# Performance work log

Measured on AMD Instinct MI355X. Metric: run time of the kernel, lower is better.

## Reference

```python
import jax, jax.numpy as jnp
import numpy as np

B, N, X, Y, W1, W2 = 2, 6, 8, 8, 8, 8
DIM, HEADS, DHEAD = 128, 4, 32
HD = HEADS * DHEAD
EPS = 1e-5


def setup_inputs() -> dict:
    key = jax.random.key(0)
    ks = jax.random.split(key, 12)
    d = {}
    d['q'] = jax.random.normal(ks[0], (B, N, X, Y, W1, W2, DIM), jnp.float32)
    d['k'] = jax.random.normal(ks[1], (B, N, X, Y, W1, W2, DIM), jnp.float32)
    d['v'] = jax.random.normal(ks[2], (B, N, X, Y, W1, W2, DIM), jnp.float32)
    d['skip'] = jax.random.normal(ks[3], (B, X, Y, W1, W2, DIM), jnp.float32)
    d['head_gate'] = jax.random.uniform(ks[4], (HEADS,), jnp.float32, 0.5, 1.5)
    # LayerNorm affine params (slightly perturbed so grads are nontrivial)
    d['ln_q_w'] = 1.0 + 0.1 * jax.random.normal(ks[5], (DIM,), jnp.float32)
    d['ln_q_b'] = jnp.zeros((DIM,), jnp.float32)
    d['ln_k_w'] = 1.0 + 0.1 * jax.random.normal(ks[6], (DIM,), jnp.float32)
    d['ln_k_b'] = jnp.zeros((DIM,), jnp.float32)
    d['ln_v_w'] = 1.0 + 0.1 * jax.random.normal(ks[7], (DIM,), jnp.float32)
    d['ln_v_b'] = jnp.zeros((DIM,), jnp.float32)
    # Linear weights, stored as (in, out) so x @ w + b
    s = 0.02
    d['wq'] = s * jax.random.normal(ks[8], (DIM, HD), jnp.float32)
    d['bq'] = jnp.zeros((HD,), jnp.float32)
    d['wk'] = s * jax.random.normal(ks[9], (DIM, HD), jnp.float32)
    d['bk'] = jnp.zeros((HD,), jnp.float32)
    d['wv'] = s * jax.random.normal(ks[10], (DIM, HD), jnp.float32)
    d['bv'] = jnp.zeros((HD,), jnp.float32)
    d['wp'] = s * jax.random.normal(ks[11], (HD, DIM), jnp.float32)
    d['bp'] = jnp.zeros((DIM,), jnp.float32)
    return d


def _ln(x, w, b):
    mu = jnp.mean(x, axis=-1, keepdims=True)
    var = jnp.mean(jnp.square(x - mu), axis=-1, keepdims=True)
    return (x - mu) * jax.lax.rsqrt(var + EPS) * w + b


def _windows(t):
    # (b, n, x, y, w1, w2, d) -> (b, x*y, n*w1*w2, d)
    b, n, x, y, w1, w2, dd = t.shape
    return t.transpose(0, 2, 3, 1, 4, 5, 6).reshape(b, x * y, n * w1 * w2, dd)


def _heads(t):
    # (b, l, t, HEADS*DHEAD) -> (b, m, l, t, DHEAD)
    b, l, tt, _ = t.shape
    return t.reshape(b, l, tt, HEADS, DHEAD).transpose(0, 3, 1, 2, 4)


def reference(q, k, v, skip, head_gate,
              ln_q_w, ln_q_b, ln_k_w, ln_k_b, ln_v_w, ln_v_b,
              wq, bq, wk, bk, wv, bv, wp, bp):
    b, n, x, y, w1, w2, _ = q.shape
    scale = DHEAD ** -0.5
    qh = _heads(_ln(_windows(q), ln_q_w, ln_q_b) @ wq + bq) * scale
    kh = _heads(_ln(_windows(k), ln_k_w, ln_k_b) @ wk + bk)
    vh = _heads(_ln(_windows(v), ln_v_w, ln_v_b) @ wv + bv)
    # per-window attention: l = x*y windows, Q = K = n*w1*w2 tokens
    dot = jnp.einsum('bmlqd,bmlkd->bmlqk', qh, kh)
    dot = dot * head_gate[None, :, None, None, None]
    att = jax.nn.softmax(dot, axis=-1)
    a = jnp.einsum('bmlqk,bmlkd->bmlqd', att, vh)
    a = a.transpose(0, 2, 3, 1, 4).reshape(b, x * y, n * w1 * w2, HD)
    out = a.reshape(b, x, y, n, w1, w2, HD).transpose(0, 3, 1, 2, 4, 5, 6)
    z = out @ wp + bp          # (b, n, x, y, w1, w2, dim)
    z = jnp.mean(z, axis=1)    # mean over agents n
    return z + skip
```

## Files before the change

kernel.cpp:

```cpp
#include <hip/hip_runtime.h>
#include <hip/hip_bf16.h>
#include <cstddef>

#define NB     2
#define NA     6
#define NWIN   64
#define NTOK   384
#define DIM    128
#define NHEADS 4
#define DHEAD  32

typedef __attribute__((ext_vector_type(8))) short short8;
typedef __attribute__((ext_vector_type(4))) float f32x4;

__device__ __forceinline__ unsigned short f2bf(float f) {
    __hip_bfloat16 h = __float2bfloat16(f);
    return *reinterpret_cast<unsigned short*>(&h);
}
__device__ __forceinline__ float bf2f(unsigned short u) {
    union { unsigned int i; float f; } x; x.i = ((unsigned int)u) << 16; return x.f;
}

__global__ __launch_bounds__(256) void wconv_kernel(
    const float* __restrict__ wq, const float* __restrict__ wk,
    const float* __restrict__ wv, const float* __restrict__ gate,
    unsigned short* __restrict__ wt)
{
    const int e = blockIdx.x * 256 + threadIdx.x;
    const int mat = e >> 14, i = e & 16383;
    const int kk = i >> 7, c = i & 127;
    const float* src = (mat == 0) ? wq : (mat == 1) ? wk : wv;
    const float s = (mat == 0) ? (0.17677669529663687f * gate[c >> 5]) : 1.0f;
    wt[(mat << 14) + c * DIM + kk] = f2bf(src[i] * s);
}

__global__ __launch_bounds__(256) void proj_kernel(
    const float* __restrict__ qx, const float* __restrict__ kx,
    const float* __restrict__ vx,
    const float* __restrict__ lnqw, const float* __restrict__ lnqb,
    const float* __restrict__ lnkw, const float* __restrict__ lnkb,
    const float* __restrict__ lnvw, const float* __restrict__ lnvb,
    const float* __restrict__ bq, const float* __restrict__ bk,
    const float* __restrict__ bv, const float* __restrict__ gate,
    const unsigned short* __restrict__ wt,
    unsigned short* __restrict__ qh, unsigned short* __restrict__ kh,
    unsigned short* __restrict__ vh)
{
    __shared__ unsigned short Wl[DIM * DIM];
    __shared__ unsigned short TB[4][16][152];

    const int bid  = blockIdx.x;
    const int mode = bid / 768;
    const int rr   = bid - mode * 768;
    const int b = rr / 384, l = (rr / 6) % NWIN, n = rr % 6;

    const float* xin  = (mode == 0) ? qx : (mode == 1) ? kx : vx;
    const float* lw   = (mode == 0) ? lnqw : (mode == 1) ? lnkw : lnvw;
    const float* lb   = (mode == 0) ? lnqb : (mode == 1) ? lnkb : lnvb;
    const float* bias = (mode == 0) ? bq : (mode == 1) ? bk : bv;
    const unsigned short* wtm = wt + (mode << 14);
    unsigned short* outp = (mode == 0) ? qh : (mode == 1) ? kh : vh;

#pragma unroll
    for (int it = 0; it < 8; ++it) {
        const int e = it * 256 + threadIdx.x;
        const int col = e >> 4, k8 = (e & 15) * 8;
        *(short8*)&Wl[col * DIM + (k8 ^ ((col & 7) << 3))] =
            *(const short8*)&wtm[col * DIM + k8];
    }

    const int wv_ = threadIdx.x >> 6, lane = threadIdx.x & 63;
    const int g = lane >> 4, qc = lane & 15;
    const int T0 = wv_ * 16;

    const float* xp = xin + ((size_t)((b * NA + n) * NWIN + l) * 64 + T0 + qc) * DIM;
    float xv[4][8];
    float s = 0.f, s2 = 0.f;
#pragma unroll
    for (int c = 0; c < 4; ++c) {
        const float4 a0 = *(const float4*)(xp + c * 32 + 8 * g);
        const float4 a1 = *(const float4*)(xp + c * 32 + 8 * g + 4);
        xv[c][0] = a0.x; xv[c][1] = a0.y; xv[c][2] = a0.z; xv[c][3] = a0.w;
        xv[c][4] = a1.x; xv[c][5] = a1.y; xv[c][6] = a1.z; xv[c][7] = a1.w;
#pragma unroll
        for (int u = 0; u < 8; ++u) { s += xv[c][u]; s2 += xv[c][u] * xv[c][u]; }
    }
    s  += __shfl_xor(s, 16);  s  += __shfl_xor(s, 32);
    s2 += __shfl_xor(s2, 16); s2 += __shfl_xor(s2, 32);
    const float mu   = s * (1.0f / 128.0f);
    const float var  = s2 * (1.0f / 128.0f) - mu * mu;
    const float rsig = rsqrtf(var + 1e-5f);

    short8 af[4];
#pragma unroll
    for (int c = 0; c < 4; ++c) {
        const float4 w0 = *(const float4*)(lw + c * 32 + 8 * g);
        const float4 w1 = *(const float4*)(lw + c * 32 + 8 * g + 4);
        const float4 b0 = *(const float4*)(lb + c * 32 + 8 * g);
        const float4 b1 = *(const float4*)(lb + c * 32 + 8 * g + 4);
        af[c][0] = (short)f2bf((xv[c][0] - mu) * rsig * w0.x + b0.x);
        af[c][1] = (short)f2bf((xv[c][1] - mu) * rsig * w0.y + b0.y);
        af[c][2] = (short)f2bf((xv[c][2] - mu) * rsig * w0.z + b0.z);
        af[c][3] = (short)f2bf((xv[c][3] - mu) * rsig * w0.w + b0.w);
        af[c][4] = (short)f2bf((xv[c][4] - mu) * rsig * w1.x + b1.x);
        af[c][5] = (short)f2bf((xv[c][5] - mu) * rsig * w1.y + b1.y);
        af[c][6] = (short)f2bf((xv[c][6] - mu) * rsig * w1.z + b1.z);
        af[c][7] = (short)f2bf((xv[c][7] - mu) * rsig * w1.w + b1.w);
    }
    __syncthreads();

    const f32x4 z = {0.f, 0.f, 0.f, 0.f};
    f32x4 accs[8];
#pragma unroll
    for (int ct = 0; ct < 8; ++ct) {
        f32x4 acc = z;
        const int col = ct * 16 + qc;
#pragma unroll
        for (int c = 0; c < 4; ++c) {
            const short8 bf = *(const short8*)&Wl[col * DIM + ((c * 32 + 8 * g) ^ ((col & 7) << 3))];
            acc = __builtin_amdgcn_mfma_f32_16x16x32_bf16(af[c], bf, acc, 0, 0, 0);
        }
        accs[ct] = acc;
    }

    if (mode == 2) {
#pragma unroll
        for (int ct = 0; ct < 8; ++ct) {
            const int col = ct * 16 + qc;
            const int head = ct >> 1;
            const int d = (ct & 1) * 16 + qc;
            const float bb = bias[col];
            const size_t hb = (size_t)(b * NHEADS + head) * NWIN + l;
            ushort4 o;
            o.x = f2bf(accs[ct][0] + bb); o.y = f2bf(accs[ct][1] + bb);
            o.z = f2bf(accs[ct][2] + bb); o.w = f2bf(accs[ct][3] + bb);
            *(ushort4*)&outp[(hb * DHEAD + d) * NTOK + n * 64 + T0 + 4 * g] = o;
        }
    } else {
        const float gs = (mode == 0) ? 0.17677669529663687f : 1.0f;
#pragma unroll
        for (int ct = 0; ct < 8; ++ct) {
            const int col = ct * 16 + qc;
            const float bb = bias[col] * ((mode == 0) ? (gs * gate[ct >> 1]) : 1.0f);
#pragma unroll
            for (int r = 0; r < 4; ++r)
                TB[wv_][4 * g + r][col] = f2bf(accs[ct][r] + bb);
        }
        const size_t hbg = (size_t)(b * NHEADS + g) * NWIN + l;
        unsigned short* dst = outp + (hbg * NTOK + n * 64 + T0 + qc) * DHEAD;
#pragma unroll
        for (int j = 0; j < 4; ++j)
            *(short8*)&dst[8 * j] = *(const short8*)&TB[wv_][qc][32 * g + 8 * j];
    }
}

__global__ __launch_bounds__(256) void attn_kernel(
    const unsigned short* __restrict__ qh, const unsigned short* __restrict__ kh,
    const unsigned short* __restrict__ vt, unsigned short* __restrict__ aout)
{
    __shared__ unsigned short P[4][3][16][40];

    const int tid  = threadIdx.x;
    const int w    = tid >> 6;
    const int lane = tid & 63;
    const int g    = lane >> 4;
    const int qc   = lane & 15;

    const int idx = blockIdx.x;
    const int b = idx >> 9, h = (idx >> 7) & 3, l = (idx >> 1) & 63, half = idx & 1;
    const size_t base = (size_t)((b * NHEADS + h) * NWIN + l) * (NTOK * DHEAD);
    const unsigned short* Qp = qh + base;
    const unsigned short* Kp = kh + base;
    const unsigned short* Vp = vt + base;

    short8 qf[3];
#pragma unroll
    for (int j = 0; j < 3; ++j)
        qf[j] = *(const short8*)(Qp + (size_t)(((half * 4 + w) * 3 + j) * 16 + qc) * DHEAD + 8 * g);

    f32x4 o0[3], o1[3];
    float psum[3];
    const f32x4 z = {0.f, 0.f, 0.f, 0.f};
#pragma unroll
    for (int j = 0; j < 3; ++j) { o0[j] = z; o1[j] = z; psum[j] = 0.f; }

    for (int kc = 0; kc < 12; ++kc) {
        const int k0 = kc * 32;
        const short8 ka0 = *(const short8*)(Kp + (size_t)(k0 + qc) * DHEAD + 8 * g);
        const short8 ka1 = *(const short8*)(Kp + (size_t)(k0 + 16 + qc) * DHEAD + 8 * g);
        const short8 vb0 = *(const short8*)(Vp + (size_t)qc * NTOK + k0 + 8 * g);
        const short8 vb1 = *(const short8*)(Vp + (size_t)(16 + qc) * NTOK + k0 + 8 * g);

#pragma unroll
        for (int j = 0; j < 3; ++j) {
            f32x4 s0 = __builtin_amdgcn_mfma_f32_16x16x32_bf16(ka0, qf[j], z, 0, 0, 0);
            f32x4 s1 = __builtin_amdgcn_mfma_f32_16x16x32_bf16(ka1, qf[j], z, 0, 0, 0);
            const float e0 = __expf(s0[0]), e1 = __expf(s0[1]), e2 = __expf(s0[2]), e3 = __expf(s0[3]);
            const float e4 = __expf(s1[0]), e5 = __expf(s1[1]), e6 = __expf(s1[2]), e7 = __expf(s1[3]);
            psum[j] += ((e0 + e1) + (e2 + e3)) + ((e4 + e5) + (e6 + e7));
            ushort4 pw0, pw1;
            pw0.x = f2bf(e0); pw0.y = f2bf(e1); pw0.z = f2bf(e2); pw0.w = f2bf(e3);
            pw1.x = f2bf(e4); pw1.y = f2bf(e5); pw1.z = f2bf(e6); pw1.w = f2bf(e7);
            *(ushort4*)&P[w][j][qc][4 * g]      = pw0;
            *(ushort4*)&P[w][j][qc][16 + 4 * g] = pw1;
        }
#pragma unroll
        for (int j = 0; j < 3; ++j) {
            const short8 pa = *(const short8*)&P[w][j][qc][8 * g];
            o0[j] = __builtin_amdgcn_mfma_f32_16x16x32_bf16(pa, vb0, o0[j], 0, 0, 0);
            o1[j] = __builtin_amdgcn_mfma_f32_16x16x32_bf16(pa, vb1, o1[j], 0, 0, 0);
        }
    }

#pragma unroll
    for (int j = 0; j < 3; ++j) {
        float ps = psum[j];
        ps += __shfl_xor(ps, 16);
        ps += __shfl_xor(ps, 32);
        const float inv = 1.0f / ps;
        const int q0 = ((half * 4 + w) * 3 + j) * 16;
        const size_t ob = ((size_t)(b * NWIN + l) * NTOK + q0) * (NHEADS * DHEAD) + h * DHEAD + qc;
#pragma unroll
        for (int r = 0; r < 4; ++r) {
            const float iv = __shfl(inv, 4 * g + r);
            aout[ob + (size_t)(4 * g + r) * (NHEADS * DHEAD)]      = f2bf(o0[j][r] * iv);
            aout[ob + (size_t)(4 * g + r) * (NHEADS * DHEAD) + 16] = f2bf(o1[j][r] * iv);
        }
    }
}

__global__ __launch_bounds__(256) void outproj_kernel(
    const unsigned short* __restrict__ a, const float* __restrict__ wp,
    const float* __restrict__ bp, const float* __restrict__ skip,
    float* __restrict__ outp)
{
    __shared__ float at[DIM * 68];
    __shared__ float wl[DIM * 64];

    const int tid = threadIdx.x;
    const int bid = blockIdx.x;
    const int b = bid >> 7, l = (bid >> 1) & 63, cg = bid & 1;
    const int c0 = cg * 64;

#pragma unroll
    for (int rep = 0; rep < 8; ++rep) {
        const int idx = rep * 256 + tid;
        const int row = idx >> 4, cc4 = idx & 15;
        *(float4*)&wl[row * 64 + cc4 * 4] = *(const float4*)&wp[row * 128 + c0 + cc4 * 4];
    }

    const size_t abase = (size_t)(b * NWIN + l) * NTOK * DIM;
#pragma unroll
    for (int r = 0; r < 32; ++r) {
        const int f = tid + 256 * r;
        const int w_ = f >> 7, d = f & 127;
        float s = 0.f;
#pragma unroll
        for (int n = 0; n < NA; ++n)
            s += bf2f(a[abase + (size_t)(n * 64 + w_) * DIM + d]);
        at[d * 68 + w_] = s * (1.0f / 6.0f);
    }
    __syncthreads();

    const int cx = tid & 15, ty = tid >> 4;
    float acc[4][4];
#pragma unroll
    for (int i = 0; i < 4; ++i)
#pragma unroll
        for (int j = 0; j < 4; ++j) acc[i][j] = 0.f;

#pragma unroll 4
    for (int i = 0; i < DIM; ++i) {
        const float4 wa = *(const float4*)&wl[i * 64 + 4 * cx];
        const float4 aa = *(const float4*)&at[i * 68 + 4 * ty];
        acc[0][0] += aa.x * wa.x; acc[0][1] += aa.x * wa.y; acc[0][2] += aa.x * wa.z; acc[0][3] += aa.x * wa.w;
        acc[1][0] += aa.y * wa.x; acc[1][1] += aa.y * wa.y; acc[1][2] += aa.y * wa.z; acc[1][3] += aa.y * wa.w;
        acc[2][0] += aa.z * wa.x; acc[2][1] += aa.z * wa.y; acc[2][2] += aa.z * wa.z; acc[2][3] += aa.z * wa.w;
        acc[3][0] += aa.w * wa.x; acc[3][1] += aa.w * wa.y; acc[3][2] += aa.w * wa.z; acc[3][3] += aa.w * wa.w;
    }

    const float4 bb = *(const float4*)&bp[c0 + 4 * cx];
#pragma unroll
    for (int u = 0; u < 4; ++u) {
        const int w_ = 4 * ty + u;
        const size_t oidx = ((size_t)(b * NWIN + l) * 64 + w_) * DIM + c0 + 4 * cx;
        const float4 sk = *(const float4*)&skip[oidx];
        float4 o;
        o.x = acc[u][0] + bb.x + sk.x;
        o.y = acc[u][1] + bb.y + sk.y;
        o.z = acc[u][2] + bb.z + sk.z;
        o.w = acc[u][3] + bb.w + sk.w;
        *(float4*)&outp[oidx] = o;
    }
}

extern "C" void kernel_launch(void* const* d_in, const int* in_sizes, int n_in,
                              void* d_out, int out_size, void* d_ws, size_t ws_size,
                              hipStream_t stream) {
    const float* q      = (const float*)d_in[0];
    const float* k      = (const float*)d_in[1];
    const float* v      = (const float*)d_in[2];
    const float* skip   = (const float*)d_in[3];
    const float* gate   = (const float*)d_in[4];
    const float* ln_q_w = (const float*)d_in[5];
    const float* ln_q_b = (const float*)d_in[6];
    const float* ln_k_w = (const float*)d_in[7];
    const float* ln_k_b = (const float*)d_in[8];
    const float* ln_v_w = (const float*)d_in[9];
    const float* ln_v_b = (const float*)d_in[10];
    const float* wq     = (const float*)d_in[11];
    const float* bq     = (const float*)d_in[12];
    const float* wk     = (const float*)d_in[13];
    const float* bk     = (const float*)d_in[14];
    const float* wv     = (const float*)d_in[15];
    const float* bv     = (const float*)d_in[16];
    const float* wp     = (const float*)d_in[17];
    const float* bp     = (const float*)d_in[18];
    float* outp = (float*)d_out;

    const size_t per = (size_t)NB * NHEADS * NWIN * NTOK * DHEAD;
    unsigned short* qh = (unsigned short*)d_ws;
    unsigned short* kh = qh + per;
    unsigned short* vh = kh + per;
    unsigned short* wt = vh + per;
    unsigned short* a  = wt + 3 * 16384;

    wconv_kernel<<<192, 256, 0, stream>>>(wq, wk, wv, gate, wt);
    proj_kernel<<<3 * NB * NWIN * NA, 256, 0, stream>>>(
        q, k, v, ln_q_w, ln_q_b, ln_k_w, ln_k_b, ln_v_w, ln_v_b,
        bq, bk, bv, gate, wt, qh, kh, vh);
    attn_kernel<<<NB * NHEADS * NWIN * 2, 256, 0, stream>>>(qh, kh, vh, a);
    outproj_kernel<<<NB * NWIN * 2, 256, 0, stream>>>(a, wp, bp, skip, outp);
}
```

Baseline: 78.18 us.

## Stream projection weights from global into registers instead of LDS staging

The projection kernel no longer stages the whole 128x128 bf16 weight matrix (32KB) into shared memory behind a block barrier. Each wave now loads its weight fragments directly from global/L2 with double-buffered register prefetch, and applies the bias epilogue per column tile so accumulators need not stay live. Launch bounds are raised to target 4 blocks per CU. This cuts LDS use and the sync, which should allow higher occupancy, at the cost of each wave reading weights redundantly from cache.

```diff
diff --git a/kernel.cpp b/kernel.cpp
--- a/kernel.cpp
+++ b/kernel.cpp
@@ -34,7 +34,7 @@
     wt[(mat << 14) + c * DIM + kk] = f2bf(src[i] * s);
 }
 
-__global__ __launch_bounds__(256) void proj_kernel(
+__global__ __launch_bounds__(256, 4) void proj_kernel(
     const float* __restrict__ qx, const float* __restrict__ kx,
     const float* __restrict__ vx,
     const float* __restrict__ lnqw, const float* __restrict__ lnqb,
@@ -46,7 +46,6 @@
     unsigned short* __restrict__ qh, unsigned short* __restrict__ kh,
     unsigned short* __restrict__ vh)
 {
-    __shared__ unsigned short Wl[DIM * DIM];
     __shared__ unsigned short TB[4][16][152];
 
     const int bid  = blockIdx.x;
@@ -60,14 +59,6 @@
     const float* bias = (mode == 0) ? bq : (mode == 1) ? bk : bv;
     const unsigned short* wtm = wt + (mode << 14);
     unsigned short* outp = (mode == 0) ? qh : (mode == 1) ? kh : vh;
-
-#pragma unroll
-    for (int it = 0; it < 8; ++it) {
-        const int e = it * 256 + threadIdx.x;
-        const int col = e >> 4, k8 = (e & 15) * 8;
-        *(short8*)&Wl[col * DIM + (k8 ^ ((col & 7) << 3))] =
-            *(const short8*)&wtm[col * DIM + k8];
-    }
 
     const int wv_ = threadIdx.x >> 6, lane = threadIdx.x & 63;
     const int g = lane >> 4, qc = lane & 15;
@@ -107,45 +98,58 @@
         af[c][6] = (short)f2bf((xv[c][6] - mu) * rsig * w1.z + b1.z);
         af[c][7] = (short)f2bf((xv[c][7] - mu) * rsig * w1.w + b1.w);
     }
-    __syncthreads();
 
     const f32x4 z = {0.f, 0.f, 0.f, 0.f};
-    f32x4 accs[8];
+    const float gs = 0.17677669529663687f;
+    short8 pipe0[4], pipe1[4];
+#pragma unroll
+    for (int c = 0; c < 4; ++c)
+        pipe0[c] = *(const short8*)&wtm[qc * DIM + c * 32 + 8 * g];
+
 #pragma unroll
     for (int ct = 0; ct < 8; ++ct) {
+        if (ct < 7) {
+            const int ncol = (ct + 1) * 16 + qc;
+            if (ct & 1) {
+#pragma unroll
+                for (int c = 0; c < 4; ++c)
+                    pipe0[c] = *(const short8*)&wtm[ncol * DIM + c * 32 + 8 * g];
+            } else {
+#pragma unroll
+                for (int c = 0; c < 4; ++c)
+                    pipe1[c] = *(const short8*)&wtm[ncol * DIM + c * 32 + 8 * g];
+            }
+        }
         f32x4 acc = z;
+        if (ct & 1) {
+#pragma unroll
+            for (int c = 0; c < 4; ++c)
+                acc = __builtin_amdgcn_mfma_f32_16x16x32_bf16(af[c], pipe1[c], acc, 0, 0, 0);
+        } else {
+#pragma unroll
+            for (int c = 0; c < 4; ++c)
+                acc = __builtin_amdgcn_mfma_f32_16x16x32_bf16(af[c], pipe0[c], acc, 0, 0, 0);
+        }
+
         const int col = ct * 16 + qc;
-#pragma unroll
-        for (int c = 0; c < 4; ++c) {
-            const short8 bf = *(const short8*)&Wl[col * DIM + ((c * 32 + 8 * g) ^ ((col & 7) << 3))];
-            acc = __builtin_amdgcn_mfma_f32_16x16x32_bf16(af[c], bf, acc, 0, 0, 0);
-        }
-        accs[ct] = acc;
-    }
-
-    if (mode == 2) {
-#pragma unroll
-        for (int ct = 0; ct < 8; ++ct) {
-            const int col = ct * 16 + qc;
+        if (mode == 2) {
             const int head = ct >> 1;
             const int d = (ct & 1) * 16 + qc;
             const float bb = bias[col];
             const size_t hb = (size_t)(b * NHEADS + head) * NWIN + l;
             ushort4 o;
-            o.x = f2bf(accs[ct][0] + bb); o.y = f2bf(accs[ct][1] + bb);
-            o.z = f2bf(accs[ct][2] + bb); o.w = f2bf(accs[ct][3] + bb);
+            o.x = f2bf(acc[0] + bb); o.y = f2bf(acc[1] + bb);
+            o.z = f2bf(acc[2] + bb); o.w = f2bf(acc[3] + bb);
             *(ushort4*)&outp[(hb * DHEAD + d) * NTOK + n * 64 + T0 + 4 * g] = o;
-        }
-    } else {
-        const float gs = (mode == 0) ? 0.17677669529663687f : 1.0f;
-#pragma unroll
-        for (int ct = 0; ct < 8; ++ct) {
-            const int col = ct * 16 + qc;
+        } else {
             const float bb = bias[col] * ((mode == 0) ? (gs * gate[ct >> 1]) : 1.0f);
 #pragma unroll
             for (int r = 0; r < 4; ++r)
-                TB[wv_][4 * g + r][col] = f2bf(accs[ct][r] + bb);
-        }
+                TB[wv_][4 * g + r][col] = f2bf(acc[r] + bb);
+        }
+    }
+
+    if (mode != 2) {
         const size_t hbg = (size_t)(b * NHEADS + g) * NWIN + l;
         unsigned short* dst = outp + (hbg * NTOK + n * 64 + T0 + qc) * DHEAD;
 #pragma unroll
```

After: 101.0 us. 29.2% more time.
